# Optimization experiments

Hardware: AMD Instinct MI355X
Metric: run time of the kernel (lower is better)

## Reference

```python
import jax, jax.numpy as jnp
import numpy as np

N = 50000
E_RAND = 800000
IN, HID, OUT = 128, 64, 40
HEADS = (2, 1, 1)
NEG_SLOPE = 0.2


def setup_inputs() -> dict:
    key = jax.random.key(0)
    ks = jax.random.split(key, 16)
    # random edges with src != dst, then append self-loops (remove+add_self_loop)
    src_r = jax.random.randint(ks[0], (E_RAND,), 0, N)
    off = jax.random.randint(ks[1], (E_RAND,), 1, N)
    dst_r = (src_r + off) % N
    loops = jnp.arange(N)
    src = jnp.concatenate([src_r, loops]).astype(jnp.int64)
    dst = jnp.concatenate([dst_r, loops]).astype(jnp.int64)
    in_feat = jax.random.normal(ks[2], (N, IN), dtype=jnp.float32)

    def lin(k, fan_in, fan_out):
        return jax.random.normal(k, (fan_in, fan_out), dtype=jnp.float32) / np.sqrt(fan_in)

    H0, H1, H2 = HEADS
    # layer 0: in=IN, out=HID, heads=H0
    W0 = lin(ks[3], IN, H0 * HID)
    al0 = jax.random.normal(ks[4], (H0, HID), dtype=jnp.float32) * 0.1
    ar0 = jax.random.normal(ks[5], (H0, HID), dtype=jnp.float32) * 0.1
    b0 = jnp.zeros((H0 * HID,), dtype=jnp.float32)
    # layer 1: in=HID*H0, out=HID, heads=H1
    W1 = lin(ks[6], HID * H0, H1 * HID)
    al1 = jax.random.normal(ks[7], (H1, HID), dtype=jnp.float32) * 0.1
    ar1 = jax.random.normal(ks[8], (H1, HID), dtype=jnp.float32) * 0.1
    b1 = jnp.zeros((H1 * HID,), dtype=jnp.float32)
    # layer 2: in=HID*H1, out=OUT, heads=H2
    W2 = lin(ks[9], HID * H1, H2 * OUT)
    al2 = jax.random.normal(ks[10], (H2, OUT), dtype=jnp.float32) * 0.1
    ar2 = jax.random.normal(ks[11], (H2, OUT), dtype=jnp.float32) * 0.1
    b2 = jnp.zeros((H2 * OUT,), dtype=jnp.float32)
    return {"in_feat": in_feat, "src": src, "dst": dst,
            "W0": W0, "al0": al0, "ar0": ar0, "b0": b0,
            "W1": W1, "al1": al1, "ar1": ar1, "b1": b1,
            "W2": W2, "al2": al2, "ar2": ar2, "b2": b2}


def _gat_layer(x, src, dst, W, al, ar, b):
    # x: [N, Fin]; W: [Fin, H*D]; al/ar: [H, D]; b: [H*D]
    H, D = al.shape
    feat = (x @ W).reshape(-1, H, D)                 # [N, H, D]
    el = jnp.sum(feat * al, axis=-1)                 # [N, H]
    er = jnp.sum(feat * ar, axis=-1)                 # [N, H]
    e = jax.nn.leaky_relu(el[src] + er[dst], NEG_SLOPE)  # [E, H]
    m = jax.ops.segment_max(e, dst, num_segments=x.shape[0])
    ee = jnp.exp(e - jax.lax.stop_gradient(m)[dst])
    s = jax.ops.segment_sum(ee, dst, num_segments=x.shape[0])
    alpha = ee / s[dst]                              # softmax over in-edges per dst
    out = jax.ops.segment_sum(feat[src] * alpha[:, :, None], dst,
                              num_segments=x.shape[0])  # [N, H, D]
    return out + b.reshape(1, H, D)


def reference(in_feat, src, dst, W0, al0, ar0, b0, W1, al1, ar1, b1, W2, al2, ar2, b2):
    h = _gat_layer(in_feat, src, dst, W0, al0, ar0, b0).reshape(in_feat.shape[0], -1)  # flatten(1)
    h = _gat_layer(h, src, dst, W1, al1, ar1, b1).mean(axis=1)                          # mean over heads
    h = _gat_layer(h, src, dst, W2, al2, ar2, b2).reshape(in_feat.shape[0], -1)         # flatten(1)
    return h
```

## Files before the change

### kernel.cpp

```cpp
#include <hip/hip_runtime.h>
#include <hip/hip_fp16.h>
#include <math.h>

#define NEG_SLOPE 0.2f


__device__ inline float2 up2(unsigned u) {
    __half2 h;
    __builtin_memcpy(&h, &u, 4);
    return __half22float2(h);
}
__device__ inline unsigned pk2(float a, float b) {
    __half2 h = __floats2half2_rn(a, b);
    unsigned u;
    __builtin_memcpy(&u, &h, 4);
    return u;
}
__device__ inline void fma8(float* acc, const uint4& v, float p) {
    float2 f;
    f = up2(v.x); acc[0] += f.x * p; acc[1] += f.y * p;
    f = up2(v.y); acc[2] += f.x * p; acc[3] += f.y * p;
    f = up2(v.z); acc[4] += f.x * p; acc[5] += f.y * p;
    f = up2(v.w); acc[6] += f.x * p; acc[7] += f.y * p;
}
__device__ inline void fma4(float4& a, const float4& w, float xs) {
    a.x += w.x * xs; a.y += w.y * xs; a.z += w.z * xs; a.w += w.w * xs;
}
__device__ inline float dot4(const float4& a, const float4& b) {
    return a.x * b.x + a.y * b.y + a.z * b.z + a.w * b.w;
}


__global__ __launch_bounds__(256) void degree_hist_rank(const int* __restrict__ dst,
                                                        int* __restrict__ deg,
                                                        int* __restrict__ rank, int E) {
    int e = blockIdx.x * blockDim.x + threadIdx.x;
    if (e < E) rank[e] = atomicAdd(&deg[dst[e]], 1);
}

__global__ __launch_bounds__(256) void scan_block_sums(const int* __restrict__ in,
                                                       int* __restrict__ partial, int n) {
    int i = blockIdx.x * 256 + threadIdx.x;
    int v = (i < n) ? in[i] : 0;
#pragma unroll
    for (int off = 32; off; off >>= 1) v += __shfl_xor(v, off);
    __shared__ int wsum[4];
    if ((threadIdx.x & 63) == 0) wsum[threadIdx.x >> 6] = v;
    __syncthreads();
    if (threadIdx.x == 0) partial[blockIdx.x] = wsum[0] + wsum[1] + wsum[2] + wsum[3];
}

__global__ __launch_bounds__(256) void scan_offsets(const int* __restrict__ partial,
                                                    int* __restrict__ partial_scan,
                                                    int* __restrict__ total_out, int nb) {
    __shared__ int buf[256];
    int t = threadIdx.x;
    int v = (t < nb) ? partial[t] : 0;
    buf[t] = v;
    __syncthreads();
    for (int off = 1; off < 256; off <<= 1) {
        int x = (t >= off) ? buf[t - off] : 0;
        __syncthreads();
        buf[t] += x;
        __syncthreads();
    }
    partial_scan[t] = buf[t] - v;
    if (t == 255) *total_out = buf[255];
}

__global__ __launch_bounds__(256) void scan_final(const int* __restrict__ in,
                                                  const int* __restrict__ partial_scan,
                                                  int* __restrict__ out, int n) {
    __shared__ int buf[256];
    int t = threadIdx.x;
    int i = blockIdx.x * 256 + t;
    int v = (i < n) ? in[i] : 0;
    buf[t] = v;
    __syncthreads();
    for (int off = 1; off < 256; off <<= 1) {
        int x = (t >= off) ? buf[t - off] : 0;
        __syncthreads();
        buf[t] += x;
        __syncthreads();
    }
    if (i < n) out[i] = partial_scan[blockIdx.x] + buf[t] - v;
}

__global__ __launch_bounds__(256) void scatter_rank(const int* __restrict__ src,
                                                    const int* __restrict__ dst,
                                                    const int* __restrict__ rank,
                                                    const int* __restrict__ row_start,
                                                    int* __restrict__ csr_src, int E) {
    int e = blockIdx.x * blockDim.x + threadIdx.x;
    if (e >= E) return;
    int d = dst[e];
    csr_src[row_start[d] + rank[e]] = src[e];
}


__global__ __launch_bounds__(256) void pad_layer2(const float* __restrict__ W2,
                                                  const float* __restrict__ al2,
                                                  const float* __restrict__ ar2,
                                                  float* __restrict__ W2p,
                                                  float* __restrict__ al2p,
                                                  float* __restrict__ ar2p) {
    int i = blockIdx.x * 256 + threadIdx.x;
    if (i < 64 * 64) {
        int r = i >> 6, c = i & 63;
        W2p[i] = (c < 40) ? W2[r * 40 + c] : 0.f;
    }
    if (i < 64) {
        al2p[i] = (i < 40) ? al2[i] : 0.f;
        ar2p[i] = (i < 40) ? ar2[i] : 0.f;
    }
}


template <int K, int M, int G, int RPG, int H, int FSTRIDE>
__global__ __launch_bounds__((M / 4) * G) void gemm_feat_lds(const float* __restrict__ x,
                                                             const float* __restrict__ W,
                                                             const float* __restrict__ al,
                                                             const float* __restrict__ ar,
                                                             __half* __restrict__ outh,
                                                             float* __restrict__ el,
                                                             float* __restrict__ er, int N) {
    constexpr int CT = M / 4;
    constexpr int NT = CT * G;
    constexpr int ROWS = G * RPG;
    constexpr int KC = 32;
    constexpr int KC4 = KC / 4;
    constexpr int NCH = K / KC;
    constexpr int LPH = 16;
    static_assert(CT % LPH == 0, "CT must be a multiple of 16");
    __shared__ float4 sx[ROWS][KC4 + 1];
    __shared__ float4 sw[KC][CT];
    const int tid = threadIdx.x;
    const int col4 = tid % CT;
    const int grp = tid / CT;
    const int h = col4 / LPH;
    const float4* __restrict__ W4 = (const float4*)W;
    const float4* __restrict__ x4 = (const float4*)x;
    const float4 av = ((const float4*)al)[col4];
    const float4 rv = ((const float4*)ar)[col4];

    for (int base = blockIdx.x * ROWS; base < N; base += gridDim.x * ROWS) {
        float4 acc[RPG];
#pragma unroll
        for (int rr = 0; rr < RPG; ++rr) acc[rr] = float4{0.f, 0.f, 0.f, 0.f};

        for (int ch = 0; ch < NCH; ++ch) {
            __syncthreads();
#pragma unroll
            for (int i = tid; i < KC * CT; i += NT)
                sw[i / CT][i % CT] = W4[(size_t)(ch * KC) * CT + i];
#pragma unroll
            for (int i = tid; i < ROWS * KC4; i += NT) {
                int r = i / KC4, c = i % KC4;
                int row = base + r;
                sx[r][c] = (row < N) ? x4[(size_t)row * (K / 4) + ch * KC4 + c]
                                     : float4{0.f, 0.f, 0.f, 0.f};
            }
            __syncthreads();
#pragma unroll
            for (int k4 = 0; k4 < KC4; ++k4) {
                float4 w0 = sw[4 * k4 + 0][col4];
                float4 w1 = sw[4 * k4 + 1][col4];
                float4 w2 = sw[4 * k4 + 2][col4];
                float4 w3 = sw[4 * k4 + 3][col4];
#pragma unroll
                for (int rr = 0; rr < RPG; ++rr) {
                    float4 xv = sx[grp * RPG + rr][k4];
                    fma4(acc[rr], w0, xv.x);
                    fma4(acc[rr], w1, xv.y);
                    fma4(acc[rr], w2, xv.z);
                    fma4(acc[rr], w3, xv.w);
                }
            }
        }
#pragma unroll
        for (int rr = 0; rr < RPG; ++rr) {
            int row = base + grp * RPG + rr;
            if (row < N) {
                uint2 pkd;
                pkd.x = pk2(acc[rr].x, acc[rr].y);
                pkd.y = pk2(acc[rr].z, acc[rr].w);
                ((uint2*)(outh + (size_t)row * FSTRIDE))[col4] = pkd;
            }
        }
#pragma unroll
        for (int rr = 0; rr < RPG; ++rr) {
            float pl = dot4(acc[rr], av);
            float pr = dot4(acc[rr], rv);
#pragma unroll
            for (int off = 1; off < LPH; off <<= 1) {
                pl += __shfl_xor(pl, off);
                pr += __shfl_xor(pr, off);
            }
            if ((col4 % LPH) == 0) {
                int row = base + grp * RPG + rr;
                if (row < N) {
                    el[(size_t)row * H + h] = pl;
                    er[(size_t)row * H + h] = pr;
                }
            }
        }
    }
}


template <int H, int D, int FSTRIDE>
__global__ __launch_bounds__(256) void gat_aggregate(const __half* __restrict__ feat,
                                                     const float* __restrict__ el,
                                                     const float* __restrict__ er,
                                                     const int* __restrict__ row_start,
                                                     const int* __restrict__ csr_src,
                                                     const float* __restrict__ bias,
                                                     float* __restrict__ out, int N) {
    constexpr int NL = (H * D) / 8;
    int dstn = (blockIdx.x * blockDim.x + threadIdx.x) >> 6;
    int lane = threadIdx.x & 63;
    if (dstn >= N) return;
    int beg = row_start[dstn], end = row_start[dstn + 1];
    int cnt = end - beg;

    float er_d[H];
#pragma unroll
    for (int h = 0; h < H; ++h) er_d[h] = er[(size_t)dstn * H + h];

    float ssum[H];
    float acc8[8];
#pragma unroll
    for (int h = 0; h < H; ++h) ssum[h] = 0.f;
#pragma unroll
    for (int i = 0; i < 8; ++i) acc8[i] = 0.f;

    const int g = lane >> 4;
    const int ln = lane & 15;

    auto gather = [&](int s_reg, const float p_reg[H], int j) {
        uint4 v[4];
#pragma unroll
        for (int t = 0; t < 4; ++t) {
            int sj = __shfl(s_reg, j + 4 * t + g);
            const uint4* fp = (const uint4*)(feat + (size_t)sj * FSTRIDE);
            v[t] = (NL == 16 || ln < NL) ? fp[ln] : uint4{0, 0, 0, 0};
        }
#pragma unroll
        for (int t = 0; t < 4; ++t) {
            int e = j + 4 * t + g;
            float pj0 = __shfl(p_reg[0], e);
            float pj;
            if constexpr (H == 2) {
                float pj1 = __shfl(p_reg[1], e);
                pj = (ln >= 8) ? pj1 : pj0;
            } else {
                pj = pj0;
            }
            fma8(acc8, v[t], pj);
        }
    };

    if (cnt <= 64) {
        int idx = beg + lane;
        bool valid = idx < end;
        int s = valid ? csr_src[idx] : csr_src[beg];
        float ev[H], m[H], p[H];
        if constexpr (H == 2) {
            float2 e2 = ((const float2*)el)[s];
            ev[0] = e2.x + er_d[0];
            ev[1] = e2.y + er_d[1];
        } else {
            ev[0] = el[s] + er_d[0];
        }
#pragma unroll
        for (int h = 0; h < H; ++h) {
            float e = ev[h];
            e = (e > 0.f) ? e : NEG_SLOPE * e;
            ev[h] = e;
            m[h] = valid ? e : -INFINITY;
        }
#pragma unroll
        for (int h = 0; h < H; ++h)
#pragma unroll
            for (int off = 32; off; off >>= 1) m[h] = fmaxf(m[h], __shfl_xor(m[h], off));
#pragma unroll
        for (int h = 0; h < H; ++h) {
            p[h] = valid ? expf(ev[h] - m[h]) : 0.f;
            ssum[h] = p[h];
        }
        for (int j = 0; j < cnt; j += 16) gather(s, p, j);
    } else {
        float m[H];
#pragma unroll
        for (int h = 0; h < H; ++h) m[h] = -INFINITY;
        for (int i = beg + lane; i < end; i += 64) {
            int s = csr_src[i];
            float ev[H];
            if constexpr (H == 2) {
                float2 e2 = ((const float2*)el)[s];
                ev[0] = e2.x + er_d[0];
                ev[1] = e2.y + er_d[1];
            } else {
                ev[0] = el[s] + er_d[0];
            }
#pragma unroll
            for (int h = 0; h < H; ++h) {
                float e = ev[h];
                e = (e > 0.f) ? e : NEG_SLOPE * e;
                m[h] = fmaxf(m[h], e);
            }
        }
#pragma unroll
        for (int h = 0; h < H; ++h)
#pragma unroll
            for (int off = 32; off; off >>= 1) m[h] = fmaxf(m[h], __shfl_xor(m[h], off));

        for (int base = beg; base < end; base += 64) {
            int idx = base + lane;
            bool valid = idx < end;
            int s = valid ? csr_src[idx] : csr_src[beg];
            float p[H];
            float ev[H];
            if constexpr (H == 2) {
                float2 e2 = ((const float2*)el)[s];
                ev[0] = e2.x + er_d[0];
                ev[1] = e2.y + er_d[1];
            } else {
                ev[0] = el[s] + er_d[0];
            }
#pragma unroll
            for (int h = 0; h < H; ++h) {
                float e = ev[h];
                e = (e > 0.f) ? e : NEG_SLOPE * e;
                p[h] = valid ? expf(e - m[h]) : 0.f;
                ssum[h] += p[h];
            }
            int ccnt = (end - base < 64) ? end - base : 64;
            for (int j = 0; j < ccnt; j += 16) gather(s, p, j);
        }
    }

#pragma unroll
    for (int h = 0; h < H; ++h)
#pragma unroll
        for (int off = 32; off; off >>= 1) ssum[h] += __shfl_xor(ssum[h], off);
#pragma unroll
    for (int i = 0; i < 8; ++i) {
        acc8[i] += __shfl_xor(acc8[i], 16);
        acc8[i] += __shfl_xor(acc8[i], 32);
    }
    if (lane < NL) {
        float inv;
        if constexpr (H == 2) inv = 1.f / ((lane >= 8) ? ssum[1] : ssum[0]);
        else inv = 1.f / ssum[0];
        float4* op = (float4*)(out + (size_t)dstn * (H * D));
        const float4* bp = (const float4*)bias;
        float4 bv0 = bp[2 * lane], bv1 = bp[2 * lane + 1];
        float4 o0, o1;
        o0.x = acc8[0] * inv + bv0.x; o0.y = acc8[1] * inv + bv0.y;
        o0.z = acc8[2] * inv + bv0.z; o0.w = acc8[3] * inv + bv0.w;
        o1.x = acc8[4] * inv + bv1.x; o1.y = acc8[5] * inv + bv1.y;
        o1.z = acc8[6] * inv + bv1.z; o1.w = acc8[7] * inv + bv1.w;
        op[2 * lane] = o0;
        op[2 * lane + 1] = o1;
    }
}


extern "C" void kernel_launch(void* const* d_in, const int* in_sizes, int n_in,
                              void* d_out, int out_size, void* d_ws, size_t ws_size,
                              hipStream_t stream) {
    const float* in_feat = (const float*)d_in[0];
    const int*   src     = (const int*)d_in[1];
    const int*   dst     = (const int*)d_in[2];
    const float* W0 = (const float*)d_in[3];
    const float* al0 = (const float*)d_in[4];
    const float* ar0 = (const float*)d_in[5];
    const float* b0 = (const float*)d_in[6];
    const float* W1 = (const float*)d_in[7];
    const float* al1 = (const float*)d_in[8];
    const float* ar1 = (const float*)d_in[9];
    const float* b1 = (const float*)d_in[10];
    const float* W2 = (const float*)d_in[11];
    const float* al2 = (const float*)d_in[12];
    const float* ar2 = (const float*)d_in[13];
    const float* b2 = (const float*)d_in[14];
    float* out = (float*)d_out;

    const int N = in_sizes[0] / 128;
    const int E = in_sizes[1];

    char* ws = (char*)d_ws;
    auto alloc = [&](size_t bytes) -> void* {
        void* p = (void*)ws;
        ws += (bytes + 255) & ~(size_t)255;
        return p;
    };
    int* deg       = (int*)alloc((size_t)N * 4);
    int* row_start = (int*)alloc((size_t)(N + 1) * 4);
    int* csr_src   = (int*)alloc((size_t)E * 4);
    int* rank      = (int*)alloc((size_t)E * 4);
    int* partial      = (int*)alloc(256 * 4);
    int* partial_scan = (int*)alloc(256 * 4);
    __half* feat   = (__half*)alloc((size_t)N * 128 * 2);
    float* el      = (float*)alloc((size_t)N * 2 * 4);
    float* er      = (float*)alloc((size_t)N * 2 * 4);
    float* h0      = (float*)alloc((size_t)N * 128 * 4);
    float* h1      = (float*)alloc((size_t)N * 64 * 4);
    float* W2p     = (float*)alloc((size_t)64 * 64 * 4);
    float* al2p    = (float*)alloc(64 * 4);
    float* ar2p    = (float*)alloc(64 * 4);

    hipMemsetAsync(deg, 0, (size_t)N * 4, stream);

    int egrid = (E + 255) / 256;
    int nb = (N + 255) / 256;

    degree_hist_rank<<<egrid, 256, 0, stream>>>(dst, deg, rank, E);
    scan_block_sums<<<nb, 256, 0, stream>>>(deg, partial, N);
    scan_offsets<<<1, 256, 0, stream>>>(partial, partial_scan, &row_start[N], nb);
    scan_final<<<nb, 256, 0, stream>>>(deg, partial_scan, row_start, N);
    scatter_rank<<<egrid, 256, 0, stream>>>(src, dst, rank, row_start, csr_src, E);
    pad_layer2<<<16, 256, 0, stream>>>(W2, al2, ar2, W2p, al2p, ar2p);

    int ngrid = (N * 64 + 255) / 256;
    int ggrid = (N + 63) / 64;

    gemm_feat_lds<128, 128, 8, 8, 2, 128><<<ggrid, 256, 0, stream>>>(in_feat, W0, al0, ar0, feat, el, er, N);
    gat_aggregate<2, 64, 128><<<ngrid, 256, 0, stream>>>(feat, el, er, row_start, csr_src, b0, h0, N);

    gemm_feat_lds<128, 64, 16, 4, 1, 64><<<ggrid, 256, 0, stream>>>(h0, W1, al1, ar1, feat, el, er, N);
    gat_aggregate<1, 64, 64><<<ngrid, 256, 0, stream>>>(feat, el, er, row_start, csr_src, b1, h1, N);

    gemm_feat_lds<64, 64, 16, 4, 1, 64><<<ggrid, 256, 0, stream>>>(h1, W2p, al2p, ar2p, feat, el, er, N);
    gat_aggregate<1, 40, 64><<<ngrid, 256, 0, stream>>>(feat, el, er, row_start, csr_src, b2, out, N);
}
```

Measured before the change: 320.6 us.

## Double-buffer feature GEMM tiles with async global-to-LDS loads

The feature-projection GEMM now stages W and x chunks straight into LDS with global_load_lds, using two LDS buffers so the next K-chunk loads while the current one is computed. This removes the register round-trip and one barrier per chunk, so load latency can overlap with FMAs. Out-of-range rows are clamped to the last row rather than zero-filled, and the padding column on the x tile is dropped, which may add LDS bank conflicts. It also relies on the compiler placing the right vmcnt waits before each barrier and on wave-contiguous LDS destinations.

```diff
diff --git a/kernel.cpp b/kernel.cpp
--- a/kernel.cpp
+++ b/kernel.cpp
@@ -3,6 +3,8 @@
 #include <math.h>
 
 #define NEG_SLOPE 0.2f
+#define AS1 __attribute__((address_space(1)))
+#define AS3 __attribute__((address_space(3)))
 
 
 __device__ inline float2 up2(unsigned u) {
@@ -130,10 +132,12 @@
     constexpr int KC = 32;
     constexpr int KC4 = KC / 4;
     constexpr int NCH = K / KC;
+    constexpr int SWN = KC * CT;
+    constexpr int SXN = ROWS * KC4;
     constexpr int LPH = 16;
-    static_assert(CT % LPH == 0, "CT must be a multiple of 16");
-    __shared__ float4 sx[ROWS][KC4 + 1];
-    __shared__ float4 sw[KC][CT];
+    static_assert(CT % LPH == 0 && SWN % NT == 0 && SXN % NT == 0, "layout");
+    __shared__ float4 sw[2][SWN];
+    __shared__ float4 sx[2][SXN];
     const int tid = threadIdx.x;
     const int col4 = tid % CT;
     const int grp = tid / CT;
@@ -148,34 +152,44 @@
 #pragma unroll
         for (int rr = 0; rr < RPG; ++rr) acc[rr] = float4{0.f, 0.f, 0.f, 0.f};
 
+        auto stage = [&](int buf, int ch) {
+#pragma unroll
+            for (int i = tid; i < SWN; i += NT) {
+                const float4* gp = W4 + (size_t)ch * SWN + i;
+                __builtin_amdgcn_global_load_lds((AS1 const void*)gp,
+                                                 (AS3 void*)&sw[buf][i], 16, 0, 0);
+            }
+#pragma unroll
+            for (int i = tid; i < SXN; i += NT) {
+                int row = base + i / KC4;
+                if (row >= N) row = N - 1;
+                const float4* gp = x4 + (size_t)row * (K / 4) + ch * KC4 + (i % KC4);
+                __builtin_amdgcn_global_load_lds((AS1 const void*)gp,
+                                                 (AS3 void*)&sx[buf][i], 16, 0, 0);
+            }
+        };
+
+        stage(0, 0);
+        __syncthreads();
         for (int ch = 0; ch < NCH; ++ch) {
-            __syncthreads();
-#pragma unroll
-            for (int i = tid; i < KC * CT; i += NT)
-                sw[i / CT][i % CT] = W4[(size_t)(ch * KC) * CT + i];
-#pragma unroll
-            for (int i = tid; i < ROWS * KC4; i += NT) {
-                int r = i / KC4, c = i % KC4;
-                int row = base + r;
-                sx[r][c] = (row < N) ? x4[(size_t)row * (K / 4) + ch * KC4 + c]
-                                     : float4{0.f, 0.f, 0.f, 0.f};
-            }
-            __syncthreads();
+            if (ch + 1 < NCH) stage((ch + 1) & 1, ch + 1);
+            const int b = ch & 1;
 #pragma unroll
             for (int k4 = 0; k4 < KC4; ++k4) {
-                float4 w0 = sw[4 * k4 + 0][col4];
-                float4 w1 = sw[4 * k4 + 1][col4];
-                float4 w2 = sw[4 * k4 + 2][col4];
-                float4 w3 = sw[4 * k4 + 3][col4];
+                float4 w0 = sw[b][(4 * k4 + 0) * CT + col4];
+                float4 w1 = sw[b][(4 * k4 + 1) * CT + col4];
+                float4 w2 = sw[b][(4 * k4 + 2) * CT + col4];
+                float4 w3 = sw[b][(4 * k4 + 3) * CT + col4];
 #pragma unroll
                 for (int rr = 0; rr < RPG; ++rr) {
-                    float4 xv = sx[grp * RPG + rr][k4];
+                    float4 xv = sx[b][(grp * RPG + rr) * KC4 + k4];
                     fma4(acc[rr], w0, xv.x);
                     fma4(acc[rr], w1, xv.y);
                     fma4(acc[rr], w2, xv.z);
                     fma4(acc[rr], w3, xv.w);
                 }
             }
+            __syncthreads();
         }
 #pragma unroll
         for (int rr = 0; rr < RPG; ++rr) {
```

After: 345.9 us. 7.9% more time.
